# Kernel optimization log

Hardware: AMD Instinct MI355X
Metric: run time of the kernel (lower is better)

Reference implementation:

```python
import jax, jax.numpy as jnp
import numpy as np

B, N, C, H = 64, 196, 768, 16
D_FF = 4 * C


def _layernorm(x, w, b, eps=1e-5):
    mu = jnp.mean(x, axis=-1, keepdims=True)
    var = jnp.mean((x - mu) ** 2, axis=-1, keepdims=True)
    return (x - mu) * jax.lax.rsqrt(var + eps) * w + b


def _rel_indices(n, dtype):
    # faithful to GPSA.get_rel_indices: [N, N, 3] = (indx, indy, indd)
    s = int(n ** 0.5)
    ind = np.arange(s)[None, :] - np.arange(s)[:, None]
    indx = np.tile(ind, (s, s))
    indy = np.repeat(np.repeat(ind, s, axis=0), s, axis=1)
    indd = indx ** 2 + indy ** 2
    return jnp.asarray(np.stack([indx, indy, indd], axis=-1), dtype=dtype)


def setup_inputs() -> dict:
    key = jax.random.key(0)
    ks = jax.random.split(key, 8)
    std = 0.02
    return {
        "x": jax.random.normal(ks[0], (B, N, C), jnp.float32),
        "norm1_w": jnp.ones((C,), jnp.float32),
        "norm1_b": jnp.zeros((C,), jnp.float32),
        "qk_w": jax.random.normal(ks[1], (2 * C, C), jnp.float32) * std,
        "v_w": jax.random.normal(ks[2], (C, C), jnp.float32) * std,
        "pos_w": jax.random.normal(ks[3], (H, 3), jnp.float32) * std,
        "pos_b": jnp.zeros((H,), jnp.float32),
        "gating": jnp.ones((H,), jnp.float32),
        "proj_w": jax.random.normal(ks[4], (C, C), jnp.float32) * std,
        "proj_b": jnp.zeros((C,), jnp.float32),
        "norm2_w": jnp.ones((C,), jnp.float32),
        "norm2_b": jnp.zeros((C,), jnp.float32),
        "fc1_w": jax.random.normal(ks[5], (D_FF, C), jnp.float32) * std,
        "fc1_b": jnp.zeros((D_FF,), jnp.float32),
        "fc2_w": jax.random.normal(ks[6], (C, D_FF), jnp.float32) * std,
        "fc2_b": jnp.zeros((C,), jnp.float32),
    }


def reference(x, norm1_w, norm1_b, qk_w, v_w, pos_w, pos_b, gating,
              proj_w, proj_b, norm2_w, norm2_b, fc1_w, fc1_b, fc2_w, fc2_b):
    b, n, c = x.shape
    h = H
    d = c // h
    scale = d ** -0.5

    # ---- GPSA attention branch ----
    xn = _layernorm(x, norm1_w, norm1_b)
    qk = xn @ qk_w.T                               # [B, N, 2C]
    q = qk[..., :c].reshape(b, n, h, d).transpose(0, 2, 1, 3)   # [B,H,N,d]
    k = qk[..., c:].reshape(b, n, h, d).transpose(0, 2, 1, 3)
    patch_score = jax.nn.softmax(
        jnp.einsum('bhnd,bhmd->bhnm', q, k) * scale, axis=-1)

    rel = _rel_indices(n, x.dtype)                 # [N, N, 3]
    pos_score = jax.nn.softmax(
        (rel @ pos_w.T + pos_b).transpose(2, 0, 1), axis=-1)    # [H, N, N]

    sig = jax.nn.sigmoid(gating)[None, :, None, None]           # [1,H,1,1]
    attn = (1.0 - sig) * patch_score + sig * pos_score[None]
    attn = attn / jnp.sum(attn, axis=-1, keepdims=True)

    v = (xn @ v_w.T).reshape(b, n, h, d).transpose(0, 2, 1, 3)  # [B,H,N,d]
    out = jnp.einsum('bhnm,bhmd->bhnd', attn, v)
    out = out.transpose(0, 2, 1, 3).reshape(b, n, c)
    out = out @ proj_w.T + proj_b
    x = x + out

    # ---- MLP branch ----
    xn2 = _layernorm(x, norm2_w, norm2_b)
    hdn = jax.nn.gelu(xn2 @ fc1_w.T + fc1_b, approximate=False)
    x = x + (hdn @ fc2_w.T + fc2_b)
    return x
```

## Files before the change

### kernel.cpp

```cpp
#include <hip/hip_runtime.h>

#define B_ 64
#define N_ 196
#define C_ 768
#define H_ 16
#define DFF_ 3072
#define M_ (B_ * N_)

typedef float f32x4 __attribute__((ext_vector_type(4)));
typedef __bf16 bf16x8 __attribute__((ext_vector_type(8)));
typedef unsigned short u16;
typedef unsigned short u16x8 __attribute__((ext_vector_type(8)));

__device__ __forceinline__ u16 f2bf(float f) {
  unsigned u = __float_as_uint(f);
  unsigned r = (u + 0x7FFFu + ((u >> 16) & 1u)) >> 16;
  return (u16)r;
}
__device__ __forceinline__ float bf2f(u16 h) {
  return __uint_as_float(((unsigned)h) << 16);
}

__device__ __forceinline__ void gload_lds16(const u16* g, u16* l) {
  typedef const __attribute__((address_space(1))) void gp_t;
  typedef __attribute__((address_space(3))) void lp_t;
  __builtin_amdgcn_global_load_lds((gp_t*)g, (lp_t*)l, 16, 0, 0);
}

__global__ __launch_bounds__(256) void fill_sentinel(float* __restrict__ out, int n) {
  for (int i = blockIdx.x * 256 + threadIdx.x; i < n; i += gridDim.x * 256)
    out[i] = 12345.0f;
}

__global__ __launch_bounds__(256) void f2b4(const float4* __restrict__ in,
                                            ushort4* __restrict__ out, int n4) {
  for (int i = blockIdx.x * 256 + threadIdx.x; i < n4; i += gridDim.x * 256) {
    float4 v = in[i];
    ushort4 o;
    o.x = f2bf(v.x); o.y = f2bf(v.y); o.z = f2bf(v.z); o.w = f2bf(v.w);
    out[i] = o;
  }
}

__global__ __launch_bounds__(256) void ln_rows(const float* __restrict__ x,
                                               const float* __restrict__ w,
                                               const float* __restrict__ b,
                                               u16* __restrict__ out) {
  const int row = blockIdx.x;
  const int t = threadIdx.x;
  const float* xr = x + (size_t)row * C_;
  float v0 = xr[t], v1 = xr[t + 256], v2 = xr[t + 512];
  float s = v0 + v1 + v2;
  float s2 = v0 * v0 + v1 * v1 + v2 * v2;
#pragma unroll
  for (int o = 32; o; o >>= 1) { s += __shfl_xor(s, o); s2 += __shfl_xor(s2, o); }
  __shared__ float rbuf[8];
  const int wid = t >> 6;
  if ((t & 63) == 0) { rbuf[wid] = s; rbuf[wid + 4] = s2; }
  __syncthreads();
  s = rbuf[0] + rbuf[1] + rbuf[2] + rbuf[3];
  s2 = rbuf[4] + rbuf[5] + rbuf[6] + rbuf[7];
  const float mu = s * (1.f / C_);
  const float inv = rsqrtf(s2 * (1.f / C_) - mu * mu + 1e-5f);
  u16* orow = out + (size_t)row * C_;
  orow[t]       = f2bf((v0 - mu) * inv * w[t]       + b[t]);
  orow[t + 256] = f2bf((v1 - mu) * inv * w[t + 256] + b[t + 256]);
  orow[t + 512] = f2bf((v2 - mu) * inv * w[t + 512] + b[t + 512]);
}

__global__ __launch_bounds__(64) void pos_softmax(const float* __restrict__ pos_w,
                                                  const float* __restrict__ pos_b,
                                                  float* __restrict__ pos) {
  const int i = blockIdx.x;
  const int h = blockIdx.y;
  const int lane = threadIdx.x;
  const float w0 = pos_w[h * 3], w1 = pos_w[h * 3 + 1], w2 = pos_w[h * 3 + 2];
  const float bb = pos_b[h];
  const int iy = i / 14, ix = i % 14;
  float lg[4];
#pragma unroll
  for (int c = 0; c < 4; ++c) {
    const int j = lane + c * 64;
    if (j < N_) {
      const int jy = j / 14, jx = j % 14;
      const float dx = (float)(jx - ix), dy = (float)(jy - iy);
      lg[c] = dx * w0 + dy * w1 + (dx * dx + dy * dy) * w2 + bb;
    } else lg[c] = -3.4e38f;
  }
  float mx = fmaxf(fmaxf(lg[0], lg[1]), fmaxf(lg[2], lg[3]));
#pragma unroll
  for (int o = 32; o; o >>= 1) mx = fmaxf(mx, __shfl_xor(mx, o));
  float sum = 0.f;
#pragma unroll
  for (int c = 0; c < 4; ++c) {
    lg[c] = (lane + c * 64 < N_) ? expf(lg[c] - mx) : 0.f;
    sum += lg[c];
  }
#pragma unroll
  for (int o = 32; o; o >>= 1) sum += __shfl_xor(sum, o);
  const float inv = 1.f / sum;
  float* prow = pos + ((size_t)h * N_ + i) * N_;
#pragma unroll
  for (int c = 0; c < 4; ++c) {
    const int j = lane + c * 64;
    if (j < N_) prow[j] = lg[c] * inv;
  }
}

#define BM 128
#define BN 128
#define BK 64

template <int EPI>
__global__ __launch_bounds__(256, 2) void gemm_bt(
    const u16* __restrict__ A, const u16* __restrict__ Bw, void* __restrict__ Cout,
    const float* __restrict__ bias, const float* __restrict__ res,
    int M, int Nn, int K) {
  __shared__ __align__(16) u16 lA[BM * BK];
  __shared__ __align__(16) u16 lB[BN * BK];
  const int t = threadIdx.x;
  const int lane = t & 63;
  const int wid = t >> 6;
  const int wr = wid >> 1, wc = wid & 1;
  const int brow = blockIdx.y * BM;
  const int bcol = blockIdx.x * BN;
  const int r16 = lane & 15;
  const int kg = lane >> 4;

  const int srow = lane >> 3;
  const int scol = (lane & 7) * 8;

  f32x4 acc[4][4] = {};

  for (int k0 = 0; k0 < K; k0 += BK) {
    __syncthreads();
#pragma unroll
    for (int i = 0; i < 4; ++i) {
      const int c = wid * 4 + i;
      const int row = c * 8 + srow;
      gload_lds16(&A[(size_t)(brow + row) * K + k0 + scol], &lA[c * 512]);
      gload_lds16(&Bw[(size_t)(bcol + row) * K + k0 + scol], &lB[c * 512]);
    }
    __syncthreads();
#pragma unroll
    for (int kk = 0; kk < 2; ++kk) {
      bf16x8 af[4], bfr[4];
#pragma unroll
      for (int m = 0; m < 4; ++m)
        af[m] = *reinterpret_cast<const bf16x8*>(
            &lA[(wr * 64 + m * 16 + r16) * BK + (kk * 4 + kg) * 8]);
#pragma unroll
      for (int n = 0; n < 4; ++n)
        bfr[n] = *reinterpret_cast<const bf16x8*>(
            &lB[(wc * 64 + n * 16 + r16) * BK + (kk * 4 + kg) * 8]);
#pragma unroll
      for (int m = 0; m < 4; ++m)
#pragma unroll
        for (int n = 0; n < 4; ++n)
          acc[m][n] = __builtin_amdgcn_mfma_f32_16x16x32_bf16(af[m], bfr[n], acc[m][n], 0, 0, 0);
    }
  }

#pragma unroll
  for (int m = 0; m < 4; ++m) {
#pragma unroll
    for (int n = 0; n < 4; ++n) {
#pragma unroll
      for (int r = 0; r < 4; ++r) {
        const int row = brow + wr * 64 + m * 16 + kg * 4 + r;
        const int col = bcol + wc * 64 + n * 16 + r16;
        const float v = acc[m][n][r];
        if (EPI == 0) {
          ((u16*)Cout)[(size_t)row * Nn + col] = f2bf(v);
        } else if (EPI == 1) {
          ((float*)Cout)[(size_t)row * Nn + col] = v + bias[col] + res[(size_t)row * Nn + col];
        } else {
          const float u = v + bias[col];
          ((u16*)Cout)[(size_t)row * Nn + col] =
              f2bf(0.5f * u * (1.f + erff(u * 0.70710678118654752f)));
        }
      }
    }
  }
}

#define PSTR 232

__global__ __launch_bounds__(256, 2) void attn_mfma(const u16* __restrict__ qkv,
                                                    const float* __restrict__ pos,
                                                    const float* __restrict__ gating,
                                                    u16* __restrict__ out) {
  const int bh = blockIdx.x;
  const int b = bh >> 4, h = bh & 15;
  __shared__ __align__(16) u16 VT[48][PSTR];
  __shared__ __align__(16) u16 P[4][16][PSTR];
  const int t = threadIdx.x, lane = t & 63, w = t >> 6;
  const int c16 = lane & 15, g = lane >> 4;

  for (int idx = t; idx < N_ * 6; idx += 256) {
    const int j = idx / 6, c8 = idx % 6;
    const u16x8 v = *reinterpret_cast<const u16x8*>(
        &qkv[((size_t)(b * N_ + j)) * 2304 + 1536 + h * 48 + c8 * 8]);
#pragma unroll
    for (int e = 0; e < 8; ++e) VT[c8 * 8 + e][j] = v[e];
  }
  for (int idx = t; idx < 48 * 18; idx += 256) {
    const int d = idx / 18, q = idx % 18;
    *reinterpret_cast<unsigned*>(&VT[d][196 + q * 2]) = 0u;
  }
  for (int idx = t; idx < 4 * 16 * 18; idx += 256) {
    const int wv = idx / (16 * 18), rr = (idx / 18) % 16, q = idx % 18;
    *reinterpret_cast<unsigned*>(&P[wv][rr][196 + q * 2]) = 0u;
  }
  __syncthreads();

  const float sig = 1.f / (1.f + __expf(-gating[h]));
  const float scale = 0.14433756729740643f;
  const float* poshp = pos + (size_t)h * N_ * N_;

  for (int mt = w; mt < 13; mt += 4) {
    bf16x8 qa0, qa1;
    {
      const int irow = mt * 16 + c16;
      const u16* qp = &qkv[((size_t)(b * N_ + irow)) * 2304 + h * 48];
      qa0 = *reinterpret_cast<const bf16x8*>(qp + g * 8);
      if (g < 2) qa1 = *reinterpret_cast<const bf16x8*>(qp + 32 + g * 8);
      else       qa1 = bf16x8{};
    }

    f32x4 s[13];
#pragma unroll
    for (int nt = 0; nt < 13; ++nt) {
      const int jrow = nt * 16 + c16;
      const u16* kp = &qkv[((size_t)(b * N_ + jrow)) * 2304 + 768 + h * 48];
      const bf16x8 kb0 = *reinterpret_cast<const bf16x8*>(kp + g * 8);
      const bf16x8 kb1 = *reinterpret_cast<const bf16x8*>(kp + 32 + g * 8);
      f32x4 acc = {};
      acc = __builtin_amdgcn_mfma_f32_16x16x32_bf16(qa0, kb0, acc, 0, 0, 0);
      acc = __builtin_amdgcn_mfma_f32_16x16x32_bf16(qa1, kb1, acc, 0, 0, 0);
      s[nt] = acc;
    }

    float mx[4] = {-3.4e38f, -3.4e38f, -3.4e38f, -3.4e38f};
#pragma unroll
    for (int nt = 0; nt < 13; ++nt)
#pragma unroll
      for (int r = 0; r < 4; ++r) {
        float v = s[nt][r];
        if (nt == 12 && c16 >= 4) v = -3.4e38f;
        s[nt][r] = v;
        mx[r] = fmaxf(mx[r], v);
      }
#pragma unroll
    for (int r = 0; r < 4; ++r)
#pragma unroll
      for (int o = 1; o < 16; o <<= 1) mx[r] = fmaxf(mx[r], __shfl_xor(mx[r], o));

    float sum[4] = {0.f, 0.f, 0.f, 0.f};
#pragma unroll
    for (int nt = 0; nt < 13; ++nt)
#pragma unroll
      for (int r = 0; r < 4; ++r) {
        const float p = __expf((s[nt][r] - mx[r]) * scale);
        s[nt][r] = p;
        sum[r] += p;
      }
#pragma unroll
    for (int r = 0; r < 4; ++r) {
#pragma unroll
      for (int o = 1; o < 16; o <<= 1) sum[r] += __shfl_xor(sum[r], o);
      sum[r] = (1.f - sig) / sum[r];
    }

    float tot[4] = {0.f, 0.f, 0.f, 0.f};
    const int i0g = mt * 16 + 4 * g;
#pragma unroll
    for (int nt = 0; nt < 13; ++nt) {
      const int j = nt * 16 + c16;
#pragma unroll
      for (int r = 0; r < 4; ++r) {
        const int i = i0g + r;
        float pv = 0.f;
        if (i < N_ && j < N_) pv = poshp[(size_t)i * N_ + j];
        float a = s[nt][r] * sum[r] + sig * pv;
        if (j >= N_) a = 0.f;
        s[nt][r] = a;
        tot[r] += a;
      }
    }
#pragma unroll
    for (int r = 0; r < 4; ++r) {
#pragma unroll
      for (int o = 1; o < 16; o <<= 1) tot[r] += __shfl_xor(tot[r], o);
      tot[r] = 1.f / tot[r];
    }

#pragma unroll
    for (int nt = 0; nt < 13; ++nt)
#pragma unroll
      for (int r = 0; r < 4; ++r)
        P[w][4 * g + r][nt * 16 + c16] = f2bf(s[nt][r] * tot[r]);

    f32x4 oacc[3] = {};
#pragma unroll
    for (int kk2 = 0; kk2 < 7; ++kk2) {
      const bf16x8 pa = *reinterpret_cast<const bf16x8*>(&P[w][c16][kk2 * 32 + g * 8]);
#pragma unroll
      for (int dt = 0; dt < 3; ++dt) {
        const bf16x8 vb = *reinterpret_cast<const bf16x8*>(&VT[dt * 16 + c16][kk2 * 32 + g * 8]);
        oacc[dt] = __builtin_amdgcn_mfma_f32_16x16x32_bf16(pa, vb, oacc[dt], 0, 0, 0);
      }
    }

#pragma unroll
    for (int dt = 0; dt < 3; ++dt)
#pragma unroll
      for (int r = 0; r < 4; ++r) {
        const int i = i0g + r;
        if (i < N_)
          out[((size_t)(b * N_ + i)) * C_ + h * 48 + dt * 16 + c16] = f2bf(oacc[dt][r]);
      }
  }
}

extern "C" void kernel_launch(void* const* d_in, const int* in_sizes, int n_in,
                              void* d_out, int out_size, void* d_ws, size_t ws_size,
                              hipStream_t stream) {
  const size_t WS_NEEDED = 151487488;
  if (ws_size < WS_NEEDED) {
    fill_sentinel<<<512, 256, 0, stream>>>((float*)d_out, out_size);
    return;
  }

  const float* x      = (const float*)d_in[0];
  const float* n1w    = (const float*)d_in[1];
  const float* n1b    = (const float*)d_in[2];
  const float* qk_w   = (const float*)d_in[3];
  const float* v_w    = (const float*)d_in[4];
  const float* pos_w  = (const float*)d_in[5];
  const float* pos_b  = (const float*)d_in[6];
  const float* gating = (const float*)d_in[7];
  const float* proj_w = (const float*)d_in[8];
  const float* proj_b = (const float*)d_in[9];
  const float* n2w    = (const float*)d_in[10];
  const float* n2b    = (const float*)d_in[11];
  const float* fc1_w  = (const float*)d_in[12];
  const float* fc1_b  = (const float*)d_in[13];
  const float* fc2_w  = (const float*)d_in[14];
  const float* fc2_b  = (const float*)d_in[15];

  char* ws = (char*)d_ws;
  u16*   xn    = (u16*)(ws + 0);
  u16*   xn2   = (u16*)(ws + 0);
  u16*   wqkv  = (u16*)(ws + 19267584);
  u16*   wproj = (u16*)(ws + 22806528);
  u16*   wfc1  = (u16*)(ws + 23986176);
  u16*   wfc2  = (u16*)(ws + 28704768);
  float* pos   = (float*)(ws + 33423360);
  float* x1    = (float*)(ws + 35881984);
  u16*   qkv   = (u16*)(ws + 74417152);
  u16*   attno = (u16*)(ws + 132219904);
  u16*   hbuf  = (u16*)(ws + 74417152);

  f2b4<<<512, 256, 0, stream>>>((const float4*)qk_w,   (ushort4*)wqkv,                (1536 * 768) / 4);
  f2b4<<<512, 256, 0, stream>>>((const float4*)v_w,    (ushort4*)(wqkv + 1536 * 768), (768 * 768) / 4);
  f2b4<<<512, 256, 0, stream>>>((const float4*)proj_w, (ushort4*)wproj,               (768 * 768) / 4);
  f2b4<<<512, 256, 0, stream>>>((const float4*)fc1_w,  (ushort4*)wfc1,                (3072 * 768) / 4);
  f2b4<<<512, 256, 0, stream>>>((const float4*)fc2_w,  (ushort4*)wfc2,                (768 * 3072) / 4);
  ln_rows<<<M_, 256, 0, stream>>>(x, n1w, n1b, xn);
  pos_softmax<<<dim3(196, 16), 64, 0, stream>>>(pos_w, pos_b, pos);
  gemm_bt<0><<<dim3(2304 / BN, M_ / BM), 256, 0, stream>>>(xn, wqkv, qkv, nullptr, nullptr, M_, 2304, 768);
  attn_mfma<<<B_ * H_, 256, 0, stream>>>(qkv, pos, gating, attno);
  gemm_bt<1><<<dim3(768 / BN, M_ / BM), 256, 0, stream>>>(attno, wproj, x1, proj_b, x, M_, 768, 768);
  ln_rows<<<M_, 256, 0, stream>>>(x1, n2w, n2b, xn2);
  gemm_bt<2><<<dim3(3072 / BN, M_ / BM), 256, 0, stream>>>(xn2, wfc1, hbuf, fc1_b, nullptr, M_, 3072, 768);
  gemm_bt<1><<<dim3(768 / BN, M_ / BM), 256, 0, stream>>>(hbuf, wfc2, (float*)d_out, fc2_b, x1, M_, 768, 3072);
}
```

Before: 524.0 us.

## Replace GEMM with 256x256 double-buffered, swizzled, phase-pipelined MFMA kernel

Replaces the 128x128 single-buffered GEMM with a 256x256-tile, 512-thread kernel. It double-buffers LDS and issues the next tile's global-to-LDS loads while the current tile's MFMAs run, using explicit vmcnt waits, barriers and setprio. LDS addresses are XOR-swizzled to avoid bank conflicts. Larger tiles raise data reuse, but they use 128KB LDS and more accumulator registers, and the small-N GEMMs (768 columns) get few blocks, which can hurt occupancy.

```diff
diff --git a/kernel.cpp b/kernel.cpp
--- a/kernel.cpp
+++ b/kernel.cpp
@@ -107,77 +107,120 @@
   }
 }
 
-#define BM 128
-#define BN 128
-#define BK 64
+
+#define DSREAD_B(TILE)                                                        \
+  {                                                                           \
+    const int pB = ((TILE) & 1) * 32768 + 16384 + (wc >> 1) * 8192;           \
+    _Pragma("unroll") for (int fc = 0; fc < 4; ++fc) {                        \
+      const int rb = (wc & 1) * 64 + fc * 16 + c16;                           \
+      _Pragma("unroll") for (int ks = 0; ks < 2; ++ks)                        \
+          bfr[fc][ks] = *reinterpret_cast<const bf16x8*>(                     \
+              &lds[pB + rb * 64 + 8 * ((4 * ks + g) ^ (rb & 7))]);            \
+    }                                                                         \
+  }
+
+#define DSREAD_A(Q, TILE)                                                     \
+  {                                                                           \
+    const int pA = ((TILE) & 1) * 32768 + wr * 8192;                          \
+    _Pragma("unroll") for (int fr2 = 0; fr2 < 2; ++fr2) {                     \
+      const int r = ((Q) * 2 + fr2) * 16 + c16;                               \
+      _Pragma("unroll") for (int ks = 0; ks < 2; ++ks)                        \
+          af[fr2][ks] = *reinterpret_cast<const bf16x8*>(                     \
+              &lds[pA + r * 64 + 8 * ((4 * ks + g) ^ (r & 7))]);              \
+    }                                                                         \
+  }
+
+#define MMAQ(Q)                                                               \
+  _Pragma("unroll") for (int fr2 = 0; fr2 < 2; ++fr2)                         \
+      _Pragma("unroll") for (int fc = 0; fc < 4; ++fc)                        \
+          _Pragma("unroll") for (int ks = 0; ks < 2; ++ks)                    \
+              acc[(Q) * 2 + fr2][fc] = __builtin_amdgcn_mfma_f32_16x16x32_bf16( \
+                  af[fr2][ks], bfr[fc][ks], acc[(Q) * 2 + fr2][fc], 0, 0, 0);
+
+#define PHASE(Q, TILE, STAGES, VMW)                                           \
+  {                                                                           \
+    if ((Q) == 0) DSREAD_B(TILE);                                             \
+    DSREAD_A(Q, TILE);                                                        \
+    STAGES;                                                                   \
+    __builtin_amdgcn_s_barrier();                                             \
+    asm volatile("s_waitcnt lgkmcnt(0)" ::: "memory");                        \
+    __builtin_amdgcn_sched_barrier(0);                                        \
+    __builtin_amdgcn_s_setprio(1);                                            \
+    MMAQ(Q);                                                                  \
+    __builtin_amdgcn_s_setprio(0);                                            \
+    VMW;                                                                      \
+    __builtin_amdgcn_s_barrier();                                             \
+  }
 
 template <int EPI>
-__global__ __launch_bounds__(256, 2) void gemm_bt(
+__global__ __launch_bounds__(512, 2) void gemm256(
     const u16* __restrict__ A, const u16* __restrict__ Bw, void* __restrict__ Cout,
     const float* __restrict__ bias, const float* __restrict__ res,
     int M, int Nn, int K) {
-  __shared__ __align__(16) u16 lA[BM * BK];
-  __shared__ __align__(16) u16 lB[BN * BK];
-  const int t = threadIdx.x;
-  const int lane = t & 63;
-  const int wid = t >> 6;
-  const int wr = wid >> 1, wc = wid & 1;
-  const int brow = blockIdx.y * BM;
-  const int bcol = blockIdx.x * BN;
-  const int r16 = lane & 15;
-  const int kg = lane >> 4;
-
+  __shared__ __align__(16) u16 lds[65536];
+  const int t = threadIdx.x, lane = t & 63, wid = t >> 6;
+  const int wr = wid >> 2, wc = wid & 3;
+  const int c16 = lane & 15, g = lane >> 4;
+  const int brow = blockIdx.y * 256, bcol = blockIdx.x * 256;
   const int srow = lane >> 3;
-  const int scol = (lane & 7) * 8;
-
-  f32x4 acc[4][4] = {};
-
-  for (int k0 = 0; k0 < K; k0 += BK) {
-    __syncthreads();
-#pragma unroll
-    for (int i = 0; i < 4; ++i) {
-      const int c = wid * 4 + i;
-      const int row = c * 8 + srow;
-      gload_lds16(&A[(size_t)(brow + row) * K + k0 + scol], &lA[c * 512]);
-      gload_lds16(&Bw[(size_t)(bcol + row) * K + k0 + scol], &lB[c * 512]);
-    }
-    __syncthreads();
-#pragma unroll
-    for (int kk = 0; kk < 2; ++kk) {
-      bf16x8 af[4], bfr[4];
-#pragma unroll
-      for (int m = 0; m < 4; ++m)
-        af[m] = *reinterpret_cast<const bf16x8*>(
-            &lA[(wr * 64 + m * 16 + r16) * BK + (kk * 4 + kg) * 8]);
-#pragma unroll
-      for (int n = 0; n < 4; ++n)
-        bfr[n] = *reinterpret_cast<const bf16x8*>(
-            &lB[(wc * 64 + n * 16 + r16) * BK + (kk * 4 + kg) * 8]);
-#pragma unroll
-      for (int m = 0; m < 4; ++m)
-#pragma unroll
-        for (int n = 0; n < 4; ++n)
-          acc[m][n] = __builtin_amdgcn_mfma_f32_16x16x32_bf16(af[m], bfr[n], acc[m][n], 0, 0, 0);
-    }
-  }
-
-#pragma unroll
-  for (int m = 0; m < 4; ++m) {
-#pragma unroll
-    for (int n = 0; n < 4; ++n) {
-#pragma unroll
-      for (int r = 0; r < 4; ++r) {
-        const int row = brow + wr * 64 + m * 16 + kg * 4 + r;
-        const int col = bcol + wc * 64 + n * 16 + r16;
-        const float v = acc[m][n][r];
+  const int scol = 8 * ((lane & 7) ^ srow);
+
+  auto stageA = [&](int tile, int h) {
+    const int p = (tile & 1) * 32768 + h * 8192;
+    const u16* gs = A + (size_t)(brow + h * 128 + wid * 8 + srow) * K + tile * 64 + scol;
+    gload_lds16(gs, &lds[p + wid * 512]);
+    gload_lds16(gs + (size_t)64 * K, &lds[p + 4096 + wid * 512]);
+  };
+  auto stageB = [&](int tile, int h) {
+    const int p = (tile & 1) * 32768 + 16384 + h * 8192;
+    const u16* gs = Bw + (size_t)(bcol + h * 128 + wid * 8 + srow) * K + tile * 64 + scol;
+    gload_lds16(gs, &lds[p + wid * 512]);
+    gload_lds16(gs + (size_t)64 * K, &lds[p + 4096 + wid * 512]);
+  };
+
+  f32x4 acc[8][4] = {};
+  bf16x8 bfr[4][2], af[2][2];
+  const int NI = K / 128;
+
+  stageB(0, 0); stageB(0, 1); stageA(0, 0); stageA(0, 1);
+  stageB(1, 0); stageB(1, 1);
+  asm volatile("s_waitcnt vmcnt(4)" ::: "memory");
+  __builtin_amdgcn_s_barrier();
+
+  for (int it = 0, u = 0; it < NI; ++it, u += 2) {
+    const bool last = (it == NI - 1);
+    PHASE(0, u, { stageA(u + 1, 0); stageA(u + 1, 1); }, {});
+    PHASE(1, u, { if (!last) stageB(u + 2, 0); }, {});
+    PHASE(2, u, { if (!last) stageB(u + 2, 1); }, {});
+    PHASE(3, u, {}, {
+      if (last) { asm volatile("s_waitcnt vmcnt(0)" ::: "memory"); }
+      else      { asm volatile("s_waitcnt vmcnt(4)" ::: "memory"); }
+    });
+    PHASE(0, u + 1, { if (!last) { stageA(u + 2, 0); stageA(u + 2, 1); } }, {});
+    PHASE(1, u + 1, { if (!last) stageB(u + 3, 0); }, {});
+    PHASE(2, u + 1, { if (!last) stageB(u + 3, 1); }, {});
+    PHASE(3, u + 1, {}, {
+      if (!last) { asm volatile("s_waitcnt vmcnt(4)" ::: "memory"); }
+    });
+  }
+
+#pragma unroll
+  for (int fr = 0; fr < 8; ++fr) {
+#pragma unroll
+    for (int fc = 0; fc < 4; ++fc) {
+#pragma unroll
+      for (int ri = 0; ri < 4; ++ri) {
+        const int row = brow + wr * 128 + fr * 16 + g * 4 + ri;
+        const int col = bcol + wc * 64 + fc * 16 + c16;
+        const float v = acc[fr][fc][ri];
         if (EPI == 0) {
           ((u16*)Cout)[(size_t)row * Nn + col] = f2bf(v);
         } else if (EPI == 1) {
           ((float*)Cout)[(size_t)row * Nn + col] = v + bias[col] + res[(size_t)row * Nn + col];
         } else {
-          const float u = v + bias[col];
+          const float u2 = v + bias[col];
           ((u16*)Cout)[(size_t)row * Nn + col] =
-              f2bf(0.5f * u * (1.f + erff(u * 0.70710678118654752f)));
+              f2bf(0.5f * u2 * (1.f + erff(u2 * 0.70710678118654752f)));
         }
       }
     }
@@ -369,10 +412,10 @@
   f2b4<<<512, 256, 0, stream>>>((const float4*)fc2_w,  (ushort4*)wfc2,                (768 * 3072) / 4);
   ln_rows<<<M_, 256, 0, stream>>>(x, n1w, n1b, xn);
   pos_softmax<<<dim3(196, 16), 64, 0, stream>>>(pos_w, pos_b, pos);
-  gemm_bt<0><<<dim3(2304 / BN, M_ / BM), 256, 0, stream>>>(xn, wqkv, qkv, nullptr, nullptr, M_, 2304, 768);
+  gemm256<0><<<dim3(2304 / 256, M_ / 256), 512, 0, stream>>>(xn, wqkv, qkv, nullptr, nullptr, M_, 2304, 768);
   attn_mfma<<<B_ * H_, 256, 0, stream>>>(qkv, pos, gating, attno);
-  gemm_bt<1><<<dim3(768 / BN, M_ / BM), 256, 0, stream>>>(attno, wproj, x1, proj_b, x, M_, 768, 768);
+  gemm256<1><<<dim3(768 / 256, M_ / 256), 512, 0, stream>>>(attno, wproj, x1, proj_b, x, M_, 768, 768);
   ln_rows<<<M_, 256, 0, stream>>>(x1, n2w, n2b, xn2);
-  gemm_bt<2><<<dim3(3072 / BN, M_ / BM), 256, 0, stream>>>(xn2, wfc1, hbuf, fc1_b, nullptr, M_, 3072, 768);
-  gemm_bt<1><<<dim3(768 / BN, M_ / BM), 256, 0, stream>>>(hbuf, wfc2, (float*)d_out, fc2_b, x1, M_, 768, 3072);
-}
+  gemm256<2><<<dim3(3072 / 256, M_ / 256), 512, 0, stream>>>(xn2, wfc1, hbuf, fc1_b, nullptr, M_, 3072, 768);
+  gemm256<1><<<dim3(768 / 256, M_ / 256), 512, 0, stream>>>(hbuf, wfc2, (float*)d_out, fc2_b, x1, M_, 768, 3072);
+}
```

After: 506.4 us. 1.03x faster.

## Double-buffer GEMM LDS with XOR swizzle; widen attention block to 8 waves

Applied to the files above, without the earlier changes.

The GEMM kernel now double-buffers its LDS tiles, issuing the next K-slice loads before the current one is computed, so each iteration needs one barrier instead of two. It also XOR-swizzles the column chunk per row to cut LDS bank conflicts on the MFMA fragment reads. The attention kernel moves from 4 to 8 waves per block, with an adjusted P stride, so its 13 query tiles are spread across more waves. The costs are twice the LDS per GEMM block, which may lower occupancy below the 2-blocks launch bound, and one block per CU for attention.

```diff
diff --git a/kernel.cpp b/kernel.cpp
--- a/kernel.cpp
+++ b/kernel.cpp
@@ -116,8 +116,7 @@
     const u16* __restrict__ A, const u16* __restrict__ Bw, void* __restrict__ Cout,
     const float* __restrict__ bias, const float* __restrict__ res,
     int M, int Nn, int K) {
-  __shared__ __align__(16) u16 lA[BM * BK];
-  __shared__ __align__(16) u16 lB[BN * BK];
+  __shared__ __align__(16) u16 lds[2][2][BM * BK];
   const int t = threadIdx.x;
   const int lane = t & 63;
   const int wid = t >> 6;
@@ -128,37 +127,49 @@
   const int kg = lane >> 4;
 
   const int srow = lane >> 3;
-  const int scol = (lane & 7) * 8;
-
-  f32x4 acc[4][4] = {};
-
-  for (int k0 = 0; k0 < K; k0 += BK) {
-    __syncthreads();
+  const int scol = 8 * ((lane & 7) ^ srow);
+
+  auto stage = [&](int buf, int k0) {
 #pragma unroll
     for (int i = 0; i < 4; ++i) {
       const int c = wid * 4 + i;
       const int row = c * 8 + srow;
-      gload_lds16(&A[(size_t)(brow + row) * K + k0 + scol], &lA[c * 512]);
-      gload_lds16(&Bw[(size_t)(bcol + row) * K + k0 + scol], &lB[c * 512]);
-    }
-    __syncthreads();
+      gload_lds16(&A[(size_t)(brow + row) * K + k0 + scol], &lds[buf][0][c * 512]);
+      gload_lds16(&Bw[(size_t)(bcol + row) * K + k0 + scol], &lds[buf][1][c * 512]);
+    }
+  };
+
+  f32x4 acc[4][4] = {};
+  const int nt = K / BK;
+
+  stage(0, 0);
+  __syncthreads();
+  int buf = 0;
+  for (int tt = 0; tt < nt; ++tt) {
+    if (tt + 1 < nt) stage(buf ^ 1, (tt + 1) * BK);
 #pragma unroll
     for (int kk = 0; kk < 2; ++kk) {
       bf16x8 af[4], bfr[4];
 #pragma unroll
-      for (int m = 0; m < 4; ++m)
+      for (int m = 0; m < 4; ++m) {
+        const int r = wr * 64 + m * 16 + r16;
         af[m] = *reinterpret_cast<const bf16x8*>(
-            &lA[(wr * 64 + m * 16 + r16) * BK + (kk * 4 + kg) * 8]);
-#pragma unroll
-      for (int n = 0; n < 4; ++n)
+            &lds[buf][0][r * BK + 8 * ((kk * 4 + kg) ^ (r & 7))]);
+      }
+#pragma unroll
+      for (int n = 0; n < 4; ++n) {
+        const int r = wc * 64 + n * 16 + r16;
         bfr[n] = *reinterpret_cast<const bf16x8*>(
-            &lB[(wc * 64 + n * 16 + r16) * BK + (kk * 4 + kg) * 8]);
+            &lds[buf][1][r * BK + 8 * ((kk * 4 + kg) ^ (r & 7))]);
+      }
 #pragma unroll
       for (int m = 0; m < 4; ++m)
 #pragma unroll
         for (int n = 0; n < 4; ++n)
           acc[m][n] = __builtin_amdgcn_mfma_f32_16x16x32_bf16(af[m], bfr[n], acc[m][n], 0, 0, 0);
     }
+    __syncthreads();
+    buf ^= 1;
   }
 
 #pragma unroll
@@ -184,32 +195,33 @@
   }
 }
 
-#define PSTR 232
-
-__global__ __launch_bounds__(256, 2) void attn_mfma(const u16* __restrict__ qkv,
+#define PSTRV 232
+#define PSTRP 228
+
+__global__ __launch_bounds__(512, 1) void attn_mfma(const u16* __restrict__ qkv,
                                                     const float* __restrict__ pos,
                                                     const float* __restrict__ gating,
                                                     u16* __restrict__ out) {
   const int bh = blockIdx.x;
   const int b = bh >> 4, h = bh & 15;
-  __shared__ __align__(16) u16 VT[48][PSTR];
-  __shared__ __align__(16) u16 P[4][16][PSTR];
+  __shared__ __align__(16) u16 VT[48][PSTRV];
+  __shared__ __align__(16) u16 P[8][16][PSTRP];
   const int t = threadIdx.x, lane = t & 63, w = t >> 6;
   const int c16 = lane & 15, g = lane >> 4;
 
-  for (int idx = t; idx < N_ * 6; idx += 256) {
+  for (int idx = t; idx < N_ * 6; idx += 512) {
     const int j = idx / 6, c8 = idx % 6;
     const u16x8 v = *reinterpret_cast<const u16x8*>(
         &qkv[((size_t)(b * N_ + j)) * 2304 + 1536 + h * 48 + c8 * 8]);
 #pragma unroll
     for (int e = 0; e < 8; ++e) VT[c8 * 8 + e][j] = v[e];
   }
-  for (int idx = t; idx < 48 * 18; idx += 256) {
+  for (int idx = t; idx < 48 * 18; idx += 512) {
     const int d = idx / 18, q = idx % 18;
     *reinterpret_cast<unsigned*>(&VT[d][196 + q * 2]) = 0u;
   }
-  for (int idx = t; idx < 4 * 16 * 18; idx += 256) {
-    const int wv = idx / (16 * 18), rr = (idx / 18) % 16, q = idx % 18;
+  for (int idx = t; idx < 8 * 16 * 16; idx += 512) {
+    const int wv = idx / (16 * 16), rr = (idx / 16) % 16, q = idx % 16;
     *reinterpret_cast<unsigned*>(&P[wv][rr][196 + q * 2]) = 0u;
   }
   __syncthreads();
@@ -218,7 +230,7 @@
   const float scale = 0.14433756729740643f;
   const float* poshp = pos + (size_t)h * N_ * N_;
 
-  for (int mt = w; mt < 13; mt += 4) {
+  for (int mt = w; mt < 13; mt += 8) {
     bf16x8 qa0, qa1;
     {
       const int irow = mt * 16 + c16;
@@ -370,7 +382,7 @@
   ln_rows<<<M_, 256, 0, stream>>>(x, n1w, n1b, xn);
   pos_softmax<<<dim3(196, 16), 64, 0, stream>>>(pos_w, pos_b, pos);
   gemm_bt<0><<<dim3(2304 / BN, M_ / BM), 256, 0, stream>>>(xn, wqkv, qkv, nullptr, nullptr, M_, 2304, 768);
-  attn_mfma<<<B_ * H_, 256, 0, stream>>>(qkv, pos, gating, attno);
+  attn_mfma<<<B_ * H_, 512, 0, stream>>>(qkv, pos, gating, attno);
   gemm_bt<1><<<dim3(768 / BN, M_ / BM), 256, 0, stream>>>(attno, wproj, x1, proj_b, x, M_, 768, 768);
   ln_rows<<<M_, 256, 0, stream>>>(x1, n2w, n2b, xn2);
   gemm_bt<2><<<dim3(3072 / BN, M_ / BM), 256, 0, stream>>>(xn2, wfc1, hbuf, fc1_b, nullptr, M_, 3072, 768);
```

Measured after the change: 536.6 us. +2.4%, slower.
